# Performance work log

Hardware: AMD Instinct MI355X
Metric: run time of the kernel (lower is better)

Reference implementation:

```python
import jax, jax.numpy as jnp
import numpy as np

N, D, C = 16384, 64, 128
MARGIN = 1.0
EPS_NORM = 1e-6   # F.normalize eps
EPS_PD = 1e-6     # F.pairwise_distance eps (added to the difference elementwise)


def setup_inputs() -> dict:
    key = jax.random.key(0)
    embeddings = jax.random.normal(key, (N, D), dtype=jnp.float32)
    labels = (jnp.arange(N) % C).astype(jnp.int32).reshape(N, 1)
    # deterministic valid positive: same label (i % C), different index
    pos_idx = ((jnp.arange(N) + C) % N).astype(jnp.int32)
    return {"embeddings": embeddings, "labels": labels, "pos_idx": pos_idx}


def reference(embeddings, labels, pos_idx):
    # L2-normalize rows (torch F.normalize: x / max(||x||, eps))
    nrm = jnp.linalg.norm(embeddings, axis=1, keepdims=True)
    e = embeddings / jnp.maximum(nrm, EPS_NORM)

    lab = labels[:, 0]
    # torch pairwise_distance computes ||x1 - x2 + eps||_2, eps added per element:
    # ||xi - xj + eps||^2 = ||xi||^2 + ||xj||^2 - 2 xi.xj + 2*eps*(sum(xi)-sum(xj)) + D*eps^2
    sq = jnp.sum(e * e, axis=1)          # [N]
    s = jnp.sum(e, axis=1)               # [N]
    gram = e @ e.T                        # [N, N]
    d2 = (sq[:, None] + sq[None, :] - 2.0 * gram
          + 2.0 * EPS_PD * (s[:, None] - s[None, :]) + D * EPS_PD * EPS_PD)
    d2 = jnp.maximum(d2, 0.0)
    dist = jnp.sqrt(jnp.maximum(d2, 1e-12))  # guard sqrt grad at 0

    # one positive per anchor: squared distance
    pos_loss = jnp.sum(d2[jnp.arange(N), pos_idx])

    # all negatives per anchor: hinge^2 on (margin - dist)
    neg_mask = lab[:, None] != lab[None, :]
    hinge = jnp.maximum(MARGIN - dist, 0.0)
    neg_loss = jnp.sum(jnp.where(neg_mask, hinge * hinge, 0.0))

    n_comparisons = N + jnp.sum(neg_mask)
    return (pos_loss + neg_loss) / n_comparisons.astype(jnp.float32)
```

## Files before the change

kernel.cpp:

```cpp
#include <hip/hip_runtime.h>
#include <hip/hip_bf16.h>

#define NN 16384
#define DD 64
#define TT 128
#define NB 64
#define NUNITS 4160
#define NBLK 1024
#define NPOSB (NN/4)
#define SCREEN_T 0.49f

constexpr float F_EPS_PD   = 1e-6f;
constexpr float F_EPS_NORM = 1e-6f;

using bf16x8 = __attribute__((ext_vector_type(8))) short;
using f32x4  = __attribute__((ext_vector_type(4))) float;
typedef __attribute__((address_space(1))) const unsigned int gu32_t;
typedef __attribute__((address_space(3))) unsigned int       lu32_t;

__device__ __forceinline__ float wave_sum_f(float v) {
    #pragma unroll
    for (int o = 32; o >= 1; o >>= 1) v += __shfl_xor(v, o);
    return v;
}

__device__ __forceinline__ int band_off(int I) { return I * (129 - I); }

__global__ __launch_bounds__(256) void norm_kernel(
    const float* __restrict__ emb, const int* __restrict__ pidx,
    float* __restrict__ u, float* __restrict__ vc,
    __hip_bfloat16* __restrict__ ebf, float* __restrict__ posP) {
    int w    = threadIdx.x >> 6;
    int row  = blockIdx.x * 4 + w;
    int lane = threadIdx.x & 63;
    int j    = pidx[row];
    float x  = emb[(size_t)row * DD + lane];
    float xj = emb[(size_t)j   * DD + lane];

    float n2  = wave_sum_f(x * x);
    float sx  = wave_sum_f(x);
    float n2j = wave_sum_f(xj * xj);
    float sxj = wave_sum_f(xj);
    float dot = wave_sum_f(x * xj);

    float m  = fmaxf(sqrtf(n2),  F_EPS_NORM);
    float mj = fmaxf(sqrtf(n2j), F_EPS_NORM);
    ebf[(size_t)row * DD + lane] = __float2bfloat16(x / m);

    __shared__ float spos[4];
    if (lane == 0) {
        float sq  = n2 / (m * m);
        float sqj = n2j / (mj * mj);
        float s   = sx / m;
        float sj  = sxj / mj;
        float g   = dot / (m * mj);
        u[row]  = sq + 2.0f * F_EPS_PD * s;
        vc[row] = sq - 2.0f * F_EPS_PD * s + (float)DD * F_EPS_PD * F_EPS_PD;
        float d2p = sq + sqj - 2.0f * g + 2.0f * F_EPS_PD * (s - sj)
                  + (float)DD * F_EPS_PD * F_EPS_PD;
        spos[w] = fmaxf(d2p, 0.0f);
    }
    __syncthreads();
    if (threadIdx.x == 0)
        posP[blockIdx.x] = spos[0] + spos[1] + spos[2] + spos[3];
}

__global__ __launch_bounds__(256, 4) void pair_kernel(
    const short* __restrict__ ebf, const float* __restrict__ u,
    const float* __restrict__ vc, const int* __restrict__ lab,
    float* __restrict__ negP) {
    __shared__ short lbs[2][8192];
    int tid  = threadIdx.x;
    int w    = tid >> 6;
    int lane = tid & 63;
    int lrow = lane & 15, lkh = lane >> 4;

    int ks = (int)(((long long)blockIdx.x * NUNITS) / NBLK);
    int ke = (int)(((long long)(blockIdx.x + 1) * NUNITS) / NBLK);

    int I = (int)((129.0f - sqrtf(16641.0f - 4.0f * (float)ks)) * 0.5f);
    I = I < 0 ? 0 : (I > NB - 1 ? NB - 1 : I);
    while (band_off(I) > ks) --I;
    while (I < NB - 1 && band_off(I + 1) <= ks) ++I;
    int tj = 2 * I + (ks - band_off(I));

    int srr  = (w & 1) * 64 + lane;
    int wsel = w >> 1;

    bf16x8 a[4][2];
    int rowbase = I * 256 + w * 64;
    float hacc = 0.0f;
    int cur = 0;

    {
        const short* bt = ebf + (size_t)tj * (128 * DD);
        #pragma unroll
        for (int q = 0; q < 4; ++q) {
            int chunk = 2 * q + wsel;
            __builtin_amdgcn_global_load_lds(
                (gu32_t*)(const void*)(bt + (size_t)srr * DD + chunk * 8),
                (lu32_t*)(void*)&lbs[0][q * 2048 + w * 512], 16, 0, 0);
        }
        #pragma unroll
        for (int s = 0; s < 4; ++s) {
            const short* ab = ebf + (size_t)(rowbase + 16 * s + lrow) * DD + lkh * 8;
            a[s][0] = *(const bf16x8*)(ab);
            a[s][1] = *(const bf16x8*)(ab + 32);
        }
    }
    __syncthreads();

    for (int k = ks; k < ke; ++k) {
        int nI = I, ntj = tj + 1;
        bool more = (k + 1 < ke);
        if (more) {
            if (ntj == TT) { nI = I + 1; ntj = 2 * nI; }
            const short* bt = ebf + (size_t)ntj * (128 * DD);
            #pragma unroll
            for (int q = 0; q < 4; ++q) {
                int chunk = 2 * q + wsel;
                __builtin_amdgcn_global_load_lds(
                    (gu32_t*)(const void*)(bt + (size_t)srr * DD + chunk * 8),
                    (lu32_t*)(void*)&lbs[cur ^ 1][q * 2048 + w * 512], 16, 0, 0);
            }
        }

        int rt = 2 * I + (w >> 1);
        float wgt = (tj == rt) ? 1.0f : ((tj > rt) ? 2.0f : 0.0f);
        if (wgt != 0.0f) {
            int bj = tj * 128;
            const short* lb = lbs[cur];
            float hp = 0.0f;
            #pragma unroll
            for (int t = 0; t < 8; ++t) {
                bf16x8 b0 = *(const bf16x8*)&lb[lkh * 1024 + (t * 16 + lrow) * 8];
                bf16x8 b1 = *(const bf16x8*)&lb[(lkh + 4) * 1024 + (t * 16 + lrow) * 8];
                f32x4 c[4];
                #pragma unroll
                for (int s = 0; s < 4; ++s) {
                    f32x4 z = {0.f, 0.f, 0.f, 0.f};
                    z = __builtin_amdgcn_mfma_f32_16x16x32_bf16(a[s][0], b0, z, 0, 0, 0);
                    z = __builtin_amdgcn_mfma_f32_16x16x32_bf16(a[s][1], b1, z, 0, 0, 0);
                    c[s] = z;
                }
                float mx = fmaxf(fmaxf(c[0][0], c[0][1]), fmaxf(c[0][2], c[0][3]));
                mx = fmaxf(mx, fmaxf(fmaxf(c[1][0], c[1][1]), fmaxf(c[1][2], c[1][3])));
                mx = fmaxf(mx, fmaxf(fmaxf(c[2][0], c[2][1]), fmaxf(c[2][2], c[2][3])));
                mx = fmaxf(mx, fmaxf(fmaxf(c[3][0], c[3][1]), fmaxf(c[3][2], c[3][3])));
                if (__any(mx > SCREEN_T)) {
                    int j = bj + t * 16 + lrow;
                    float vj = vc[j]; int lj = lab[j];
                    #pragma unroll
                    for (int s = 0; s < 4; ++s) {
                        #pragma unroll
                        for (int r = 0; r < 4; ++r) {
                            int i0 = rowbase + 16 * s + lkh * 4 + r;
                            float d2 = fmaf(-2.0f, c[s][r], u[i0] + vj);
                            float d  = sqrtf(fmaxf(d2, 1e-12f));
                            float h  = fmaxf(1.0f - d, 0.0f);
                            if (lab[i0] != lj) hp = fmaf(h, h, hp);
                        }
                    }
                }
            }
            hacc = fmaf(wgt, hp, hacc);
        }

        __syncthreads();
        cur ^= 1;
        if (more && nI != I) {
            rowbase = nI * 256 + w * 64;
            #pragma unroll
            for (int s = 0; s < 4; ++s) {
                const short* ab = ebf + (size_t)(rowbase + 16 * s + lrow) * DD + lkh * 8;
                a[s][0] = *(const bf16x8*)(ab);
                a[s][1] = *(const bf16x8*)(ab + 32);
            }
        }
        I = nI; tj = ntj;
    }

    hacc = wave_sum_f(hacc);
    float* sred = (float*)lbs;
    if (lane == 0) sred[w] = hacc;
    __syncthreads();
    if (tid == 0)
        negP[blockIdx.x] = sred[0] + sred[1] + sred[2] + sred[3];
}

__global__ __launch_bounds__(256) void reduce_kernel(
    const float* __restrict__ posP, const float* __restrict__ negP,
    const int* __restrict__ lab, float* __restrict__ out) {
    __shared__ unsigned int hist[1024];
    int t = threadIdx.x;
    for (int i = t; i < 1024; i += 256) hist[i] = 0u;
    __syncthreads();
    const int4* lab4 = (const int4*)lab;
    for (int i = t; i < NN / 4; i += 256) {
        int4 v = lab4[i];
        atomicAdd(&hist[v.x & 1023], 1u);
        atomicAdd(&hist[v.y & 1023], 1u);
        atomicAdd(&hist[v.z & 1023], 1u);
        atomicAdd(&hist[v.w & 1023], 1u);
    }
    __syncthreads();

    float ps = 0.f, ns = 0.f;
    unsigned int sqc = 0u;
    const float4* posP4 = (const float4*)posP;
    for (int i = t; i < NPOSB / 4; i += 256) {
        float4 v = posP4[i];
        ps += (v.x + v.y) + (v.z + v.w);
    }
    for (int i = t; i < NBLK; i += 256) ns += negP[i];
    for (int i = t; i < 1024; i += 256) { unsigned int h = hist[i]; sqc += h * h; }

    ps = wave_sum_f(ps);
    ns = wave_sum_f(ns);
    #pragma unroll
    for (int o = 32; o >= 1; o >>= 1) sqc += __shfl_xor(sqc, o);

    __shared__ float sp[4], sn[4];
    __shared__ unsigned int sc[4];
    int w = t >> 6, lane = t & 63;
    if (lane == 0) { sp[w] = ps; sn[w] = ns; sc[w] = sqc; }
    __syncthreads();
    if (t == 0) {
        float pos = sp[0] + sp[1] + sp[2] + sp[3];
        float neg = sn[0] + sn[1] + sn[2] + sn[3];
        unsigned long long s2 = (unsigned long long)sc[0] + sc[1] + sc[2] + sc[3];
        unsigned long long nneg = (unsigned long long)NN * NN - s2;
        float ncomp = (float)((unsigned long long)NN + nneg);
        out[0] = (pos + neg) / ncomp;
    }
}

extern "C" void kernel_launch(void* const* d_in, const int* in_sizes, int n_in,
                              void* d_out, int out_size, void* d_ws, size_t ws_size,
                              hipStream_t stream) {
    const float* emb = (const float*)d_in[0];
    const int* lab   = (const int*)d_in[1];
    const int* pidx  = (const int*)d_in[2];
    float* out = (float*)d_out;
    char* ws = (char*)d_ws;
    float*          u    = (float*)(ws);
    float*          vc   = (float*)(ws + 65536);
    __hip_bfloat16* ebf  = (__hip_bfloat16*)(ws + 131072);
    float*          posP = (float*)(ws + 2228224);
    float*          negP = (float*)(ws + 2244608);

    norm_kernel<<<NPOSB, 256, 0, stream>>>(emb, pidx, u, vc, ebf, posP);
    pair_kernel<<<NBLK, 256, 0, stream>>>((const short*)ebf, u, vc, lab, negP);
    reduce_kernel<<<1, 256, 0, stream>>>(posP, negP, lab, out);
}
```

Measured before the change: 61.62 us.

## Use 512-row anchor bands with 3-slot swizzled LDS ring and packed v/label

Each pair-kernel block now has 8 waves covering 512 anchor rows per band instead of 256, so each staged B tile is reused by twice as many rows. The double buffer becomes a 3-slot ring with explicit vmcnt waits and raw barriers, which lets the prefetch run two tiles ahead. LDS tiles are stored row-major with an XOR swizzle to avoid bank conflicts. Per-row u and labels are hoisted into registers, and the column v value and label are packed into a float2 that norm_kernel writes, so the screened epilogue does fewer scattered loads. The cost is more registers per thread, a float compare on labels, and a changed work partition across 768 blocks.

```diff
diff --git a/kernel.cpp b/kernel.cpp
--- a/kernel.cpp
+++ b/kernel.cpp
@@ -3,11 +3,11 @@
 
 #define NN 16384
 #define DD 64
-#define TT 128
-#define NB 64
-#define NUNITS 4160
-#define NBLK 1024
+#define NBI 32
+#define NUNITS 2112
+#define NBLK 768
 #define NPOSB (NN/4)
+#define RING 3
 #define SCREEN_T 0.49f
 
 constexpr float F_EPS_PD   = 1e-6f;
@@ -24,12 +24,13 @@
     return v;
 }
 
-__device__ __forceinline__ int band_off(int I) { return I * (129 - I); }
+__device__ __forceinline__ int band_off(int I) { return 2 * I * (65 - I); }
 
 __global__ __launch_bounds__(256) void norm_kernel(
     const float* __restrict__ emb, const int* __restrict__ pidx,
-    float* __restrict__ u, float* __restrict__ vc,
-    __hip_bfloat16* __restrict__ ebf, float* __restrict__ posP) {
+    const int* __restrict__ lab, float* __restrict__ u,
+    float2* __restrict__ vcp, __hip_bfloat16* __restrict__ ebf,
+    float* __restrict__ posP) {
     int w    = threadIdx.x >> 6;
     int row  = blockIdx.x * 4 + w;
     int lane = threadIdx.x & 63;
@@ -54,8 +55,10 @@
         float s   = sx / m;
         float sj  = sxj / mj;
         float g   = dot / (m * mj);
-        u[row]  = sq + 2.0f * F_EPS_PD * s;
-        vc[row] = sq - 2.0f * F_EPS_PD * s + (float)DD * F_EPS_PD * F_EPS_PD;
+        u[row] = sq + 2.0f * F_EPS_PD * s;
+        vcp[row] = make_float2(
+            sq - 2.0f * F_EPS_PD * s + (float)DD * F_EPS_PD * F_EPS_PD,
+            (float)lab[row]);
         float d2p = sq + sqj - 2.0f * g + 2.0f * F_EPS_PD * (s - sj)
                   + (float)DD * F_EPS_PD * F_EPS_PD;
         spos[w] = fmaxf(d2p, 0.0f);
@@ -65,127 +68,129 @@
         posP[blockIdx.x] = spos[0] + spos[1] + spos[2] + spos[3];
 }
 
-__global__ __launch_bounds__(256, 4) void pair_kernel(
+__device__ __forceinline__ void stage_tile(const short* tbase, short* slot,
+                                           int w, int lane) {
+    int rlo = lane >> 3;
+    int g   = (lane & 7) ^ rlo;
+    #pragma unroll
+    for (int q = 0; q < 2; ++q) {
+        int m = w * 2 + q;
+        __builtin_amdgcn_global_load_lds(
+            (gu32_t*)(const void*)(tbase + (size_t)(8 * m + rlo) * DD + g * 8),
+            (lu32_t*)(void*)(slot + m * 512), 16, 0, 0);
+    }
+}
+
+__global__ __launch_bounds__(512, 4) void pair_kernel(
     const short* __restrict__ ebf, const float* __restrict__ u,
-    const float* __restrict__ vc, const int* __restrict__ lab,
-    float* __restrict__ negP) {
-    __shared__ short lbs[2][8192];
+    const float2* __restrict__ vcp, float* __restrict__ negP) {
+    __shared__ short ring[RING][8192];
+    __shared__ float sred[8];
     int tid  = threadIdx.x;
     int w    = tid >> 6;
     int lane = tid & 63;
     int lrow = lane & 15, lkh = lane >> 4;
+    int c0s  = ((lkh)     ^ (lrow & 7)) * 8;
+    int c1s  = ((lkh + 4) ^ (lrow & 7)) * 8;
 
     int ks = (int)(((long long)blockIdx.x * NUNITS) / NBLK);
     int ke = (int)(((long long)(blockIdx.x + 1) * NUNITS) / NBLK);
 
-    int I = (int)((129.0f - sqrtf(16641.0f - 4.0f * (float)ks)) * 0.5f);
-    I = I < 0 ? 0 : (I > NB - 1 ? NB - 1 : I);
+    int I = (int)((65.0f - sqrtf(4225.0f - 2.0f * (float)ks)) * 0.5f);
+    I = I < 0 ? 0 : (I > NBI - 1 ? NBI - 1 : I);
     while (band_off(I) > ks) --I;
-    while (I < NB - 1 && band_off(I + 1) <= ks) ++I;
-    int tj = 2 * I + (ks - band_off(I));
-
-    int srr  = (w & 1) * 64 + lane;
-    int wsel = w >> 1;
-
-    bf16x8 a[4][2];
-    int rowbase = I * 256 + w * 64;
+    while (I < NBI - 1 && band_off(I + 1) <= ks) ++I;
+
     float hacc = 0.0f;
-    int cur = 0;
-
-    {
-        const short* bt = ebf + (size_t)tj * (128 * DD);
-        #pragma unroll
-        for (int q = 0; q < 4; ++q) {
-            int chunk = 2 * q + wsel;
-            __builtin_amdgcn_global_load_lds(
-                (gu32_t*)(const void*)(bt + (size_t)srr * DD + chunk * 8),
-                (lu32_t*)(void*)&lbs[0][q * 2048 + w * 512], 16, 0, 0);
-        }
+    int k0 = ks;
+    while (k0 < ke) {
+        int bend = band_off(I + 1);
+        int n    = (ke < bend ? ke : bend) - k0;
+        int tj0  = 4 * I + (k0 - band_off(I));
+        int rowbase = I * 512 + w * 64;
+        int rt      = 4 * I + (w >> 1);
+
+        bf16x8 a[4][2];
+        float uo[4][4], lo[4][4];
         #pragma unroll
         for (int s = 0; s < 4; ++s) {
             const short* ab = ebf + (size_t)(rowbase + 16 * s + lrow) * DD + lkh * 8;
             a[s][0] = *(const bf16x8*)(ab);
             a[s][1] = *(const bf16x8*)(ab + 32);
-        }
-    }
-    __syncthreads();
-
-    for (int k = ks; k < ke; ++k) {
-        int nI = I, ntj = tj + 1;
-        bool more = (k + 1 < ke);
-        if (more) {
-            if (ntj == TT) { nI = I + 1; ntj = 2 * nI; }
-            const short* bt = ebf + (size_t)ntj * (128 * DD);
             #pragma unroll
-            for (int q = 0; q < 4; ++q) {
-                int chunk = 2 * q + wsel;
-                __builtin_amdgcn_global_load_lds(
-                    (gu32_t*)(const void*)(bt + (size_t)srr * DD + chunk * 8),
-                    (lu32_t*)(void*)&lbs[cur ^ 1][q * 2048 + w * 512], 16, 0, 0);
+            for (int r = 0; r < 4; ++r) {
+                int i0 = rowbase + 16 * s + lkh * 4 + r;
+                uo[s][r] = u[i0];
+                lo[s][r] = vcp[i0].y;
             }
         }
-
-        int rt = 2 * I + (w >> 1);
-        float wgt = (tj == rt) ? 1.0f : ((tj > rt) ? 2.0f : 0.0f);
-        if (wgt != 0.0f) {
-            int bj = tj * 128;
-            const short* lb = lbs[cur];
-            float hp = 0.0f;
-            #pragma unroll
-            for (int t = 0; t < 8; ++t) {
-                bf16x8 b0 = *(const bf16x8*)&lb[lkh * 1024 + (t * 16 + lrow) * 8];
-                bf16x8 b1 = *(const bf16x8*)&lb[(lkh + 4) * 1024 + (t * 16 + lrow) * 8];
-                f32x4 c[4];
+        int np = n < 2 ? n : 2;
+        for (int p = 0; p < np; ++p)
+            stage_tile(ebf + (size_t)(tj0 + p) * (128 * DD), &ring[p][0], w, lane);
+
+        for (int k = 0; k < n; ++k) {
+            if (k + 1 < n) asm volatile("s_waitcnt vmcnt(2)" ::: "memory");
+            else           asm volatile("s_waitcnt vmcnt(0)" ::: "memory");
+            __builtin_amdgcn_s_barrier();
+            __builtin_amdgcn_sched_barrier(0);
+            if (k + 2 < n)
+                stage_tile(ebf + (size_t)(tj0 + k + 2) * (128 * DD),
+                           &ring[(k + 2) % RING][0], w, lane);
+
+            int tj = tj0 + k;
+            float wgt = (tj == rt) ? 1.0f : ((tj > rt) ? 2.0f : 0.0f);
+            if (wgt != 0.0f) {
+                const short* sl = &ring[k % RING][0];
+                int bj = tj * 128;
+                float hp = 0.0f;
                 #pragma unroll
-                for (int s = 0; s < 4; ++s) {
-                    f32x4 z = {0.f, 0.f, 0.f, 0.f};
-                    z = __builtin_amdgcn_mfma_f32_16x16x32_bf16(a[s][0], b0, z, 0, 0, 0);
-                    z = __builtin_amdgcn_mfma_f32_16x16x32_bf16(a[s][1], b1, z, 0, 0, 0);
-                    c[s] = z;
-                }
-                float mx = fmaxf(fmaxf(c[0][0], c[0][1]), fmaxf(c[0][2], c[0][3]));
-                mx = fmaxf(mx, fmaxf(fmaxf(c[1][0], c[1][1]), fmaxf(c[1][2], c[1][3])));
-                mx = fmaxf(mx, fmaxf(fmaxf(c[2][0], c[2][1]), fmaxf(c[2][2], c[2][3])));
-                mx = fmaxf(mx, fmaxf(fmaxf(c[3][0], c[3][1]), fmaxf(c[3][2], c[3][3])));
-                if (__any(mx > SCREEN_T)) {
-                    int j = bj + t * 16 + lrow;
-                    float vj = vc[j]; int lj = lab[j];
+                for (int t = 0; t < 8; ++t) {
+                    const short* rowp = sl + (t * 16 + lrow) * 64;
+                    bf16x8 b0 = *(const bf16x8*)(rowp + c0s);
+                    bf16x8 b1 = *(const bf16x8*)(rowp + c1s);
+                    f32x4 c[4];
                     #pragma unroll
                     for (int s = 0; s < 4; ++s) {
+                        f32x4 z = {0.f, 0.f, 0.f, 0.f};
+                        z = __builtin_amdgcn_mfma_f32_16x16x32_bf16(a[s][0], b0, z, 0, 0, 0);
+                        z = __builtin_amdgcn_mfma_f32_16x16x32_bf16(a[s][1], b1, z, 0, 0, 0);
+                        c[s] = z;
+                    }
+                    float mx = fmaxf(fmaxf(c[0][0], c[0][1]), fmaxf(c[0][2], c[0][3]));
+                    mx = fmaxf(mx, fmaxf(fmaxf(c[1][0], c[1][1]), fmaxf(c[1][2], c[1][3])));
+                    mx = fmaxf(mx, fmaxf(fmaxf(c[2][0], c[2][1]), fmaxf(c[2][2], c[2][3])));
+                    mx = fmaxf(mx, fmaxf(fmaxf(c[3][0], c[3][1]), fmaxf(c[3][2], c[3][3])));
+                    if (__any(mx > SCREEN_T)) {
+                        float2 vl = vcp[bj + t * 16 + lrow];
                         #pragma unroll
-                        for (int r = 0; r < 4; ++r) {
-                            int i0 = rowbase + 16 * s + lkh * 4 + r;
-                            float d2 = fmaf(-2.0f, c[s][r], u[i0] + vj);
-                            float d  = sqrtf(fmaxf(d2, 1e-12f));
-                            float h  = fmaxf(1.0f - d, 0.0f);
-                            if (lab[i0] != lj) hp = fmaf(h, h, hp);
+                        for (int s = 0; s < 4; ++s) {
+                            #pragma unroll
+                            for (int r = 0; r < 4; ++r) {
+                                float d2 = fmaf(-2.0f, c[s][r], uo[s][r] + vl.x);
+                                float d  = sqrtf(fmaxf(d2, 1e-12f));
+                                float h  = fmaxf(1.0f - d, 0.0f);
+                                if (lo[s][r] != vl.y) hp = fmaf(h, h, hp);
+                            }
                         }
                     }
                 }
-            }
-            hacc = fmaf(wgt, hp, hacc);
-        }
-
-        __syncthreads();
-        cur ^= 1;
-        if (more && nI != I) {
-            rowbase = nI * 256 + w * 64;
-            #pragma unroll
-            for (int s = 0; s < 4; ++s) {
-                const short* ab = ebf + (size_t)(rowbase + 16 * s + lrow) * DD + lkh * 8;
-                a[s][0] = *(const bf16x8*)(ab);
-                a[s][1] = *(const bf16x8*)(ab + 32);
+                hacc = fmaf(wgt, hp, hacc);
             }
         }
-        I = nI; tj = ntj;
+        __builtin_amdgcn_s_barrier();
+        k0 += n;
+        ++I;
     }
 
     hacc = wave_sum_f(hacc);
-    float* sred = (float*)lbs;
     if (lane == 0) sred[w] = hacc;
     __syncthreads();
-    if (tid == 0)
-        negP[blockIdx.x] = sred[0] + sred[1] + sred[2] + sred[3];
+    if (tid == 0) {
+        float tn = 0.f;
+        #pragma unroll
+        for (int i = 0; i < 8; ++i) tn += sred[i];
+        negP[blockIdx.x] = tn;
+    }
 }
 
 __global__ __launch_bounds__(256) void reduce_kernel(
@@ -244,12 +249,12 @@
     float* out = (float*)d_out;
     char* ws = (char*)d_ws;
     float*          u    = (float*)(ws);
-    float*          vc   = (float*)(ws + 65536);
-    __hip_bfloat16* ebf  = (__hip_bfloat16*)(ws + 131072);
-    float*          posP = (float*)(ws + 2228224);
-    float*          negP = (float*)(ws + 2244608);
-
-    norm_kernel<<<NPOSB, 256, 0, stream>>>(emb, pidx, u, vc, ebf, posP);
-    pair_kernel<<<NBLK, 256, 0, stream>>>((const short*)ebf, u, vc, lab, negP);
+    float2*         vcp  = (float2*)(ws + 65536);
+    __hip_bfloat16* ebf  = (__hip_bfloat16*)(ws + 196608);
+    float*          posP = (float*)(ws + 2293760);
+    float*          negP = (float*)(ws + 2310144);
+
+    norm_kernel<<<NPOSB, 256, 0, stream>>>(emb, pidx, lab, u, vcp, ebf, posP);
+    pair_kernel<<<NBLK, 512, 0, stream>>>((const short*)ebf, u, vcp, negP);
     reduce_kernel<<<1, 256, 0, stream>>>(posP, negP, lab, out);
 }
```

After: 57.96 us. -5.9%, faster.
